# Optimization experiments

Measured on AMD Instinct MI355X. Metric: run time of the kernel, lower is better.

## Reference

```python
import jax, jax.numpy as jnp
import numpy as np

HID = 3584; NH = 16; NKV = 8; HD = 256; S = 3072; WIN = 2048
SOFTCAP = 50.0; QSCALE = 256.0 ** -0.5  # query_pre_attn_scalar = 256
NEG = -2.3819763e38


def _rope(x, cos, sin):
    # x: (B, S, heads, HD); cos/sin: (S, HD//2). Gemma half-split complex RoPE.
    x1, x2 = jnp.split(x, 2, axis=-1)
    c = cos[None, :, None, :]
    s = sin[None, :, None, :]
    return jnp.concatenate([x1 * c - x2 * s, x1 * s + x2 * c], axis=-1)


def setup_inputs() -> dict:
    key = jax.random.key(0)
    k1, k2, k3 = jax.random.split(key, 3)
    hidden_states = jax.random.normal(k1, (1, S, HID), jnp.float32)
    qkv_w = jax.random.normal(k2, (NH * HD + 2 * NKV * HD, HID), jnp.float32) * 0.02
    o_w = jax.random.normal(k3, (HID, NH * HD), jnp.float32) * 0.02
    inv = 1.0 / (10000.0 ** (jnp.arange(0, HD, 2, dtype=jnp.float32) / HD))
    ang = jnp.arange(S, dtype=jnp.float32)[:, None] * inv[None, :]
    freqs_cis = jnp.stack([jnp.cos(ang), jnp.sin(ang)], axis=-1)  # (S, HD//2, 2)
    kv_write_indices = jnp.arange(S, dtype=jnp.int32)
    k_cache = jnp.zeros((1, S, NKV, HD), jnp.float32)
    v_cache = jnp.zeros((1, S, NKV, HD), jnp.float32)
    i = jnp.arange(S)[:, None]
    j = jnp.arange(S)[None, :]
    mask = jnp.where(j <= i, 0.0, NEG).astype(jnp.float32)[None, None]  # causal (1,1,S,S)
    return dict(hidden_states=hidden_states, freqs_cis=freqs_cis,
                kv_write_indices=kv_write_indices, k_cache=k_cache, v_cache=v_cache,
                mask=mask, qkv_w=qkv_w, o_w=o_w)


def reference(hidden_states, freqs_cis, kv_write_indices, k_cache, v_cache, mask, qkv_w, o_w):
    B, L, _ = hidden_states.shape
    qkv = hidden_states @ qkv_w.T  # (B, L, 8192)
    xq, xk, xv = jnp.split(qkv, [NH * HD, NH * HD + NKV * HD], axis=-1)
    xq = xq.reshape(B, L, NH, HD)
    xk = xk.reshape(B, L, NKV, HD)
    xv = xv.reshape(B, L, NKV, HD)
    cos, sin = freqs_cis[..., 0], freqs_cis[..., 1]
    xq = _rope(xq, cos, sin)
    xk = _rope(xk, cos, sin)
    # KV cache index_copy_ on dim 1
    k_all = k_cache.at[:, kv_write_indices].set(xk)  # (B, T, NKV, HD)
    v_all = v_cache.at[:, kv_write_indices].set(xv)
    T = k_all.shape[1]
    G = NH // NKV  # queries per kv head; grouped einsum avoids repeat_interleave
    q = (xq * QSCALE).transpose(0, 2, 1, 3).reshape(B, NKV, G, L, HD)
    k = k_all.transpose(0, 2, 1, 3)  # (B, NKV, T, HD)
    v = v_all.transpose(0, 2, 1, 3)
    scores = jnp.einsum('bkgsd,bktd->bkgst', q, k)
    # logit softcapping
    scores = jnp.tanh(scores / SOFTCAP) * SOFTCAP
    # sliding-window band applied on top of the provided (causal) mask
    i = jnp.arange(L)[:, None]
    j = jnp.arange(T)[None, :]
    band = (j >= i - WIN + 1) & (j <= i + WIN - 1)
    m = jnp.where(band, mask, NEG)  # (1,1,L,T)
    scores = scores + m[:, :, None]  # broadcast over group dim
    probs = jax.nn.softmax(scores.astype(jnp.float32), axis=-1).astype(q.dtype)
    out = jnp.einsum('bkgst,bktd->bkgsd', probs, v)
    out = out.reshape(B, NH, L, HD).transpose(0, 2, 1, 3).reshape(B, L, NH * HD)
    return out @ o_w.T
```

## Files before the change

kernel.cpp:

```cpp
#include <hip/hip_runtime.h>

#define S_LEN 3072
#define NHQ 16
#define NKVH 8
#define HDIM 256
#define WIN 2048
#define QKV_COLS 8192

typedef __bf16 bf16x8 __attribute__((ext_vector_type(8)));
typedef float f32x4 __attribute__((ext_vector_type(4)));

__device__ __forceinline__ unsigned short f2bf(float f) {
    union { float f; unsigned u; } v; v.f = f;
    unsigned r = v.u + 0x7FFFu + ((v.u >> 16) & 1u);
    return (unsigned short)(r >> 16);
}
__device__ __forceinline__ float bf2f(unsigned short u) {
    union { unsigned u; float f; } v; v.u = ((unsigned)u) << 16; return v.f;
}

typedef __attribute__((address_space(3))) void lds_void_t;
typedef const __attribute__((address_space(1))) void glb_void_t;
__device__ __forceinline__ void async16(const void* g, void* l) {
    __builtin_amdgcn_global_load_lds((glb_void_t*)g, (lds_void_t*)l, 16, 0, 0);
}

__global__ __launch_bounds__(256) void cast_bf16_kernel(const float* __restrict__ src,
                                                        unsigned short* __restrict__ dst,
                                                        int n) {
    int i = (blockIdx.x * 256 + threadIdx.x) * 4;
    if (i >= n) return;
    float4 v = *(const float4*)(src + i);
    ushort4 o;
    o.x = f2bf(v.x); o.y = f2bf(v.y); o.z = f2bf(v.z); o.w = f2bf(v.w);
    *(ushort4*)(dst + i) = o;
}

template <int OUT_BF16>
__global__ __launch_bounds__(256) void gemm_bt(const unsigned short* __restrict__ A,
                                               const unsigned short* __restrict__ B,
                                               void* __restrict__ Cv,
                                               int N, int K) {
    __shared__ __align__(16) unsigned short At[128 * 32];
    __shared__ __align__(16) unsigned short Bt[128 * 32];
    const int tid = threadIdx.x;
    const int wid = tid >> 6, lane = tid & 63;
    const int ln = lane & 15, quad = lane >> 4;
    const int bm = blockIdx.y, bn = blockIdx.x;
    const int wm = wid >> 1, wn = wid & 1;

    const f32x4 fzero = {0.f, 0.f, 0.f, 0.f};
    f32x4 acc[4][4];
#pragma unroll
    for (int i = 0; i < 4; i++) {
#pragma unroll
        for (int j = 0; j < 4; j++) acc[i][j] = fzero;
    }

    const unsigned short* gA = A + (size_t)(bm * 128 + wid * 32 + (lane >> 2)) * K + (lane & 3) * 8;
    const unsigned short* gB = B + (size_t)(bn * 128 + wid * 32 + (lane >> 2)) * K + (lane & 3) * 8;
    unsigned short* lA = At + wid * 32 * 32;
    unsigned short* lB = Bt + wid * 32 * 32;

    for (int k0 = 0; k0 < K; k0 += 32) {
        async16(gA + k0, lA);
        async16(gA + k0 + 16 * K, lA + 16 * 32);
        async16(gB + k0, lB);
        async16(gB + k0 + 16 * K, lB + 16 * 32);
        __syncthreads();

        bf16x8 af[4], bfr[4];
#pragma unroll
        for (int mt = 0; mt < 4; mt++)
            af[mt] = *(const bf16x8*)(At + (wm * 64 + mt * 16 + ln) * 32 + quad * 8);
#pragma unroll
        for (int nt = 0; nt < 4; nt++)
            bfr[nt] = *(const bf16x8*)(Bt + (wn * 64 + nt * 16 + ln) * 32 + quad * 8);
#pragma unroll
        for (int mt = 0; mt < 4; mt++) {
#pragma unroll
            for (int nt = 0; nt < 4; nt++)
                acc[mt][nt] = __builtin_amdgcn_mfma_f32_16x16x32_bf16(af[mt], bfr[nt], acc[mt][nt], 0, 0, 0);
        }
        __syncthreads();
    }

    const int row0 = bm * 128 + wm * 64 + quad * 4;
    const int col0 = bn * 128 + wn * 64 + ln;
    if (OUT_BF16) {
        unsigned short* C = (unsigned short*)Cv;
#pragma unroll
        for (int mt = 0; mt < 4; mt++) {
#pragma unroll
            for (int nt = 0; nt < 4; nt++) {
#pragma unroll
                for (int rr = 0; rr < 4; rr++)
                    C[(size_t)(row0 + mt * 16 + rr) * N + col0 + nt * 16] = f2bf(acc[mt][nt][rr]);
            }
        }
    } else {
        float* C = (float*)Cv;
#pragma unroll
        for (int mt = 0; mt < 4; mt++) {
#pragma unroll
            for (int nt = 0; nt < 4; nt++) {
#pragma unroll
                for (int rr = 0; rr < 4; rr++)
                    C[(size_t)(row0 + mt * 16 + rr) * N + col0 + nt * 16] = acc[mt][nt][rr];
            }
        }
    }
}

__global__ __launch_bounds__(256) void rope_kernel(const unsigned short* __restrict__ qkv,
                                                   const float* __restrict__ freqs,
                                                   const int* __restrict__ kvidx,
                                                   unsigned short* __restrict__ Qb,
                                                   unsigned short* __restrict__ Kb) {
    int t = blockIdx.x * 256 + threadIdx.x;
    int d = t & 127;
    int t2 = t >> 7;
    int hh = t2 % 24;
    int pos = t2 / 24;
    if (pos >= S_LEN) return;
    float2 cs = *(const float2*)(freqs + ((size_t)pos * 128 + d) * 2);
    if (hh < NHQ) {
        const unsigned short* src = qkv + (size_t)pos * QKV_COLS + hh * HDIM + d;
        float x1 = bf2f(src[0]), x2 = bf2f(src[128]);
        float o1 = (x1 * cs.x - x2 * cs.y) * 0.0625f;
        float o2 = (x1 * cs.y + x2 * cs.x) * 0.0625f;
        unsigned short* dst = Qb + ((size_t)hh * S_LEN + pos) * HDIM + d;
        dst[0] = f2bf(o1);
        dst[128] = f2bf(o2);
    } else {
        int kvh = hh - NHQ;
        const unsigned short* src = qkv + (size_t)pos * QKV_COLS + NHQ * HDIM + kvh * HDIM + d;
        float x1 = bf2f(src[0]), x2 = bf2f(src[128]);
        float o1 = x1 * cs.x - x2 * cs.y;
        float o2 = x1 * cs.y + x2 * cs.x;
        int wpos = kvidx[pos];
        unsigned short* dst = Kb + ((size_t)kvh * S_LEN + wpos) * HDIM + d;
        dst[0] = f2bf(o1);
        dst[128] = f2bf(o2);
    }
}

__global__ __launch_bounds__(256) void vtrans_kernel(const unsigned short* __restrict__ qkv,
                                                     const int* __restrict__ kvidx,
                                                     unsigned short* __restrict__ Vbt) {
    __shared__ unsigned short T[64][72];
    int pos0 = blockIdx.x * 64;
    int c0 = blockIdx.y * 64;
    int a = threadIdx.x >> 6;
    int b = threadIdx.x & 63;
#pragma unroll
    for (int r = 0; r < 16; r++) {
        int pl = r * 4 + a;
        T[pl][b] = qkv[(size_t)(pos0 + pl) * QKV_COLS + 6144 + c0 + b];
    }
    __syncthreads();
    int wpos = kvidx[pos0 + b];
#pragma unroll
    for (int r = 0; r < 16; r++) {
        int cl = r * 4 + a;
        Vbt[(size_t)(c0 + cl) * S_LEN + wpos] = T[b][cl];
    }
}

__global__ __launch_bounds__(256) void attn_kernel(const unsigned short* __restrict__ Qb,
                                                   const unsigned short* __restrict__ Kb,
                                                   const unsigned short* __restrict__ Vbt,
                                                   float* __restrict__ Acc,
                                                   float* __restrict__ Ps,
                                                   unsigned short* __restrict__ attn_out) {
    __shared__ __align__(16) unsigned short Kl[32][264];
    __shared__ __align__(16) unsigned short Vt[256][40];
    __shared__ __align__(16) unsigned short Pl[4][16][40];

    const int h = blockIdx.x / 96;
    const int it = 95 - (blockIdx.x % 96);
    int qb, sub, nc;
    if (it < 16)      { qb = it; sub = 0; nc = 1; }
    else if (it < 48) { int e = it - 16; qb = 16 + (e >> 1); sub = e & 1; nc = 2; }
    else              { int e = it - 48; qb = 32 + e / 3; sub = e % 3; nc = 3; }

    const int kv = h >> 1;
    const int q0 = qb * 64;
    const int tid = threadIdx.x;
    const int wid = tid >> 6, lane = tid & 63;
    const int ln = lane & 15, quad = lane >> 4;

    bf16x8 qf[8];
    {
        const unsigned short* qrow = Qb + ((size_t)h * S_LEN + q0 + wid * 16 + ln) * HDIM;
#pragma unroll
        for (int k0 = 0; k0 < 8; k0++)
            qf[k0] = *(const bf16x8*)(qrow + k0 * 32 + quad * 8);
    }

    const f32x4 fzero = {0.f, 0.f, 0.f, 0.f};
    f32x4 acc[16];
#pragma unroll
    for (int t = 0; t < 16; t++) acc[t] = fzero;
    float ps[4] = {0.f, 0.f, 0.f, 0.f};

    const int imin = q0 + wid * 16;
    const int imax = imin + 15;
    const int irow = imin + quad * 4;

    const int t_lo = (q0 >= WIN) ? ((q0 - (WIN - 1)) >> 5) : 0;
    const int t_hi = (q0 + 63) >> 5;
    const int tn = t_hi - t_lo + 1;
    const int ts = t_lo + (tn * sub) / nc;
    const int te = t_lo + (tn * (sub + 1)) / nc;

    const int krow = tid >> 3, kcs = (tid & 7) * 32;
    const unsigned short* ksrc0 = Kb + ((size_t)kv * S_LEN + krow) * HDIM + kcs;
    const unsigned short* vsrc0 = Vbt + ((size_t)kv * HDIM + tid) * S_LEN;

    for (int tt = ts; tt < te; tt++) {
        const int p0 = tt * 32;
        {
            const unsigned short* ks = ksrc0 + (size_t)p0 * HDIM;
            unsigned short* kd = &Kl[krow][kcs];
#pragma unroll
            for (int j = 0; j < 4; j++)
                *(uint4*)(kd + j * 8) = *(const uint4*)(ks + j * 8);
            const unsigned short* vs = vsrc0 + p0;
            unsigned short* vd = &Vt[tid][0];
#pragma unroll
            for (int j = 0; j < 4; j++)
                *(uint4*)(vd + j * 8) = *(const uint4*)(vs + j * 8);
        }
        __syncthreads();

        const bool live = (p0 <= imax) && (p0 + 31 >= imin - WIN + 1);
        if (live) {
            f32x4 s0 = fzero, s1 = fzero;
#pragma unroll
            for (int k0 = 0; k0 < 8; k0++) {
                bf16x8 b0 = *(const bf16x8*)(&Kl[ln][k0 * 32 + quad * 8]);
                s0 = __builtin_amdgcn_mfma_f32_16x16x32_bf16(qf[k0], b0, s0, 0, 0, 0);
            }
#pragma unroll
            for (int k0 = 0; k0 < 8; k0++) {
                bf16x8 b1 = *(const bf16x8*)(&Kl[16 + ln][k0 * 32 + quad * 8]);
                s1 = __builtin_amdgcn_mfma_f32_16x16x32_bf16(qf[k0], b1, s1, 0, 0, 0);
            }

            const bool full = (p0 + 31 <= imin) && (p0 >= imax - WIN + 1);
#pragma unroll
            for (int r = 0; r < 4; r++) {
                float z0 = __expf(s0[r] * 0.04f);
                float z1 = __expf(s1[r] * 0.04f);
                float t0 = fmaf(-100.f, __builtin_amdgcn_rcpf(z0 + 1.f), 50.f);
                float t1 = fmaf(-100.f, __builtin_amdgcn_rcpf(z1 + 1.f), 50.f);
                float p0v = __expf(t0);
                float p1v = __expf(t1);
                if (!full) {
                    const int i = irow + r;
                    int j0 = p0 + ln, j1 = p0 + 16 + ln;
                    p0v = ((j0 <= i) && (j0 + WIN > i)) ? p0v : 0.f;
                    p1v = ((j1 <= i) && (j1 + WIN > i)) ? p1v : 0.f;
                }
                ps[r] += p0v + p1v;
                Pl[wid][quad * 4 + r][ln] = f2bf(p0v);
                Pl[wid][quad * 4 + r][16 + ln] = f2bf(p1v);
            }
            bf16x8 pa = *(const bf16x8*)(&Pl[wid][ln][quad * 8]);
#pragma unroll
            for (int t = 0; t < 16; t++) {
                bf16x8 vb = *(const bf16x8*)(&Vt[t * 16 + ln][quad * 8]);
                acc[t] = __builtin_amdgcn_mfma_f32_16x16x32_bf16(pa, vb, acc[t], 0, 0, 0);
            }
        }
        __syncthreads();
    }

    float psr[4];
#pragma unroll
    for (int r = 0; r < 4; r++) {
        float s = ps[r];
#pragma unroll
        for (int o = 1; o <= 8; o <<= 1)
            s += __shfl_xor(s, o);
        psr[r] = s;
    }

    if (nc == 1) {
#pragma unroll
        for (int t = 0; t < 16; t++) {
#pragma unroll
            for (int r = 0; r < 4; r++) {
                float o = acc[t][r] * __builtin_amdgcn_rcpf(psr[r]);
                attn_out[(size_t)(irow + r) * 4096 + h * HDIM + t * 16 + ln] = f2bf(o);
            }
        }
    } else {
        if (ln == 0) {
#pragma unroll
            for (int r = 0; r < 4; r++)
                atomicAdd(&Ps[h * S_LEN + irow + r], psr[r]);
        }
#pragma unroll
        for (int t = 0; t < 16; t++) {
#pragma unroll
            for (int r = 0; r < 4; r++)
                atomicAdd(&Acc[((size_t)h * S_LEN + irow + r) * HDIM + t * 16 + ln], acc[t][r]);
        }
    }
}

__global__ __launch_bounds__(256) void norm_kernel(const float* __restrict__ Acc,
                                                   const float* __restrict__ Ps,
                                                   unsigned short* __restrict__ attn_out) {
    int row = blockIdx.x * 4 + (threadIdx.x >> 6);
    int lane = threadIdx.x & 63;
    int h = row >> 11;
    int pos = 1024 + (row & 2047);
    float4 a = *(const float4*)(Acc + ((size_t)h * S_LEN + pos) * HDIM + lane * 4);
    float inv = __builtin_amdgcn_rcpf(Ps[h * S_LEN + pos]);
    ushort4 o;
    o.x = f2bf(a.x * inv); o.y = f2bf(a.y * inv);
    o.z = f2bf(a.z * inv); o.w = f2bf(a.w * inv);
    *(ushort4*)(attn_out + (size_t)pos * 4096 + h * HDIM + lane * 4) = o;
}

extern "C" void kernel_launch(void* const* d_in, const int* in_sizes, int n_in,
                              void* d_out, int out_size, void* d_ws, size_t ws_size,
                              hipStream_t stream) {
    (void)in_sizes; (void)n_in; (void)out_size; (void)ws_size;
    const float* hidden = (const float*)d_in[0];
    const float* freqs  = (const float*)d_in[1];
    const int* kvidx    = (const int*)d_in[2];
    const float* qkv_w  = (const float*)d_in[6];
    const float* o_w    = (const float*)d_in[7];
    float* out = (float*)d_out;

    char* ws = (char*)d_ws;
    unsigned short* hs_bf   = (unsigned short*)(ws);
    unsigned short* w1_bf   = (unsigned short*)(ws + 22020096);
    unsigned short* w2_bf   = (unsigned short*)(ws + 80740352);
    unsigned short* qkv_bf  = (unsigned short*)(ws + 110100480);
    unsigned short* Qb      = (unsigned short*)(ws + 160432128);
    unsigned short* Kb      = (unsigned short*)(ws + 185597952);
    unsigned short* Vbt     = (unsigned short*)(ws + 198180864);
    unsigned short* attn_bf = (unsigned short*)(ws + 210763776);

    float* Acc = (float*)(ws + 110100480);
    float* Ps  = (float*)(ws);

    cast_bf16_kernel<<<10752, 256, 0, stream>>>(hidden, hs_bf, 11010048);
    cast_bf16_kernel<<<28672, 256, 0, stream>>>(qkv_w, w1_bf, 29360128);
    cast_bf16_kernel<<<14336, 256, 0, stream>>>(o_w, w2_bf, 14680064);

    gemm_bt<1><<<dim3(64, 24), 256, 0, stream>>>(hs_bf, w1_bf, (void*)qkv_bf, 8192, 3584);

    rope_kernel<<<36864, 256, 0, stream>>>(qkv_bf, freqs, kvidx, Qb, Kb);
    vtrans_kernel<<<dim3(48, 32), 256, 0, stream>>>(qkv_bf, kvidx, Vbt);

    hipMemsetAsync(Acc, 0, (size_t)16 * 3072 * 256 * 4, stream);
    hipMemsetAsync(Ps, 0, (size_t)16 * 3072 * 4, stream);

    attn_kernel<<<1536, 256, 0, stream>>>(Qb, Kb, Vbt, Acc, Ps, attn_bf);
    norm_kernel<<<8192, 256, 0, stream>>>(Acc, Ps, attn_bf);

    gemm_bt<0><<<dim3(28, 24), 256, 0, stream>>>(attn_bf, w2_bf, (void*)out, 3584, 4096);
}
```

Measured before the change: 949.9 us.

## Share KV tiles across GQA head pair and double-buffer async LDS loads

The attention kernel now runs 512 threads per block so both query heads of a KV group share one K/V tile load, halving the block count and global K/V traffic. K/V tiles are fetched with async global-to-LDS loads into a double buffer, so the next tile's fetch overlaps the current tile's MFMA work and one barrier per iteration is removed. XOR swizzled LDS layouts replace the padded arrays to avoid bank conflicts. Larger blocks and the launch-bounds hint may reduce occupancy or raise register pressure.

New measurement: 943.2 us. About the same (-0.7%).

```diff
diff --git a/kernel.cpp b/kernel.cpp
--- a/kernel.cpp
+++ b/kernel.cpp
@@ -167,32 +167,33 @@
     }
 }
 
-__global__ __launch_bounds__(256) void attn_kernel(const unsigned short* __restrict__ Qb,
-                                                   const unsigned short* __restrict__ Kb,
-                                                   const unsigned short* __restrict__ Vbt,
-                                                   float* __restrict__ Acc,
-                                                   float* __restrict__ Ps,
-                                                   unsigned short* __restrict__ attn_out) {
-    __shared__ __align__(16) unsigned short Kl[32][264];
-    __shared__ __align__(16) unsigned short Vt[256][40];
-    __shared__ __align__(16) unsigned short Pl[4][16][40];
-
-    const int h = blockIdx.x / 96;
+__global__ __launch_bounds__(512, 4) void attn_kernel(const unsigned short* __restrict__ Qb,
+                                                      const unsigned short* __restrict__ Kb,
+                                                      const unsigned short* __restrict__ Vbt,
+                                                      float* __restrict__ Acc,
+                                                      float* __restrict__ Ps,
+                                                      unsigned short* __restrict__ attn_out) {
+    __shared__ __align__(16) unsigned short Kl[2][32 * 256];
+    __shared__ __align__(16) unsigned short Vl[2][256 * 32];
+    __shared__ __align__(16) unsigned short Plb[8][16][40];
+
+    const int kv = blockIdx.x / 96;
     const int it = 95 - (blockIdx.x % 96);
     int qb, sub, nc;
     if (it < 16)      { qb = it; sub = 0; nc = 1; }
     else if (it < 48) { int e = it - 16; qb = 16 + (e >> 1); sub = e & 1; nc = 2; }
     else              { int e = it - 48; qb = 32 + e / 3; sub = e % 3; nc = 3; }
 
-    const int kv = h >> 1;
     const int q0 = qb * 64;
     const int tid = threadIdx.x;
     const int wid = tid >> 6, lane = tid & 63;
     const int ln = lane & 15, quad = lane >> 4;
+    const int h = kv * 2 + (wid >> 2);
+    const int wrow = (wid & 3) * 16;
 
     bf16x8 qf[8];
     {
-        const unsigned short* qrow = Qb + ((size_t)h * S_LEN + q0 + wid * 16 + ln) * HDIM;
+        const unsigned short* qrow = Qb + ((size_t)h * S_LEN + q0 + wrow + ln) * HDIM;
 #pragma unroll
         for (int k0 = 0; k0 < 8; k0++)
             qf[k0] = *(const bf16x8*)(qrow + k0 * 32 + quad * 8);
@@ -204,7 +205,7 @@
     for (int t = 0; t < 16; t++) acc[t] = fzero;
     float ps[4] = {0.f, 0.f, 0.f, 0.f};
 
-    const int imin = q0 + wid * 16;
+    const int imin = q0 + wrow;
     const int imax = imin + 15;
     const int irow = imin + quad * 4;
 
@@ -214,37 +215,55 @@
     const int ts = t_lo + (tn * sub) / nc;
     const int te = t_lo + (tn * (sub + 1)) / nc;
 
-    const int krow = tid >> 3, kcs = (tid & 7) * 32;
-    const unsigned short* ksrc0 = Kb + ((size_t)kv * S_LEN + krow) * HDIM + kcs;
-    const unsigned short* vsrc0 = Vbt + ((size_t)kv * HDIM + tid) * S_LEN;
+    const unsigned short* kSrcA = Kb + ((size_t)kv * S_LEN + (tid >> 5)) * HDIM
+                                  + ((tid & 31) ^ ((tid >> 5) & 7)) * 8;
+    const unsigned short* vSrcA = Vbt + ((size_t)kv * HDIM + (tid >> 2)) * S_LEN
+                                  + ((tid & 3) ^ ((tid >> 3) & 3)) * 8;
+
+    {
+        const int p0s = ts * 32;
+        const unsigned short* ks = kSrcA + (size_t)p0s * HDIM;
+        const unsigned short* vs = vSrcA + p0s;
+        async16(ks,                 &Kl[0][tid * 8]);
+        async16(ks + 16 * HDIM,     &Kl[0][(512 + tid) * 8]);
+        async16(vs,                 &Vl[0][tid * 8]);
+        async16(vs + 128 * S_LEN,   &Vl[0][(512 + tid) * 8]);
+    }
+
+    const int kswz = (ln & 7);
+    const unsigned short* vbb_off = (const unsigned short*)0; (void)vbb_off;
+    int cur = 0;
 
     for (int tt = ts; tt < te; tt++) {
+        asm volatile("s_waitcnt vmcnt(0)" ::: "memory");
+        __builtin_amdgcn_s_barrier();
+        asm volatile("" ::: "memory");
+
+        if (tt + 1 < te) {
+            const int p0n = (tt + 1) * 32;
+            const unsigned short* ks = kSrcA + (size_t)p0n * HDIM;
+            const unsigned short* vs = vSrcA + p0n;
+            async16(ks,                 &Kl[cur ^ 1][tid * 8]);
+            async16(ks + 16 * HDIM,     &Kl[cur ^ 1][(512 + tid) * 8]);
+            async16(vs,                 &Vl[cur ^ 1][tid * 8]);
+            async16(vs + 128 * S_LEN,   &Vl[cur ^ 1][(512 + tid) * 8]);
+        }
+
         const int p0 = tt * 32;
-        {
-            const unsigned short* ks = ksrc0 + (size_t)p0 * HDIM;
-            unsigned short* kd = &Kl[krow][kcs];
-#pragma unroll
-            for (int j = 0; j < 4; j++)
-                *(uint4*)(kd + j * 8) = *(const uint4*)(ks + j * 8);
-            const unsigned short* vs = vsrc0 + p0;
-            unsigned short* vd = &Vt[tid][0];
-#pragma unroll
-            for (int j = 0; j < 4; j++)
-                *(uint4*)(vd + j * 8) = *(const uint4*)(vs + j * 8);
-        }
-        __syncthreads();
-
         const bool live = (p0 <= imax) && (p0 + 31 >= imin - WIN + 1);
         if (live) {
+            const unsigned short* kb = Kl[cur];
             f32x4 s0 = fzero, s1 = fzero;
 #pragma unroll
             for (int k0 = 0; k0 < 8; k0++) {
-                bf16x8 b0 = *(const bf16x8*)(&Kl[ln][k0 * 32 + quad * 8]);
+                const int cp = (((k0 * 4 + quad) ^ kswz) << 3);
+                bf16x8 b0 = *(const bf16x8*)(kb + ln * HDIM + cp);
                 s0 = __builtin_amdgcn_mfma_f32_16x16x32_bf16(qf[k0], b0, s0, 0, 0, 0);
             }
 #pragma unroll
             for (int k0 = 0; k0 < 8; k0++) {
-                bf16x8 b1 = *(const bf16x8*)(&Kl[16 + ln][k0 * 32 + quad * 8]);
+                const int cp = (((k0 * 4 + quad) ^ kswz) << 3);
+                bf16x8 b1 = *(const bf16x8*)(kb + (16 + ln) * HDIM + cp);
                 s1 = __builtin_amdgcn_mfma_f32_16x16x32_bf16(qf[k0], b1, s1, 0, 0, 0);
             }
 
@@ -264,17 +283,18 @@
                     p1v = ((j1 <= i) && (j1 + WIN > i)) ? p1v : 0.f;
                 }
                 ps[r] += p0v + p1v;
-                Pl[wid][quad * 4 + r][ln] = f2bf(p0v);
-                Pl[wid][quad * 4 + r][16 + ln] = f2bf(p1v);
-            }
-            bf16x8 pa = *(const bf16x8*)(&Pl[wid][ln][quad * 8]);
+                Plb[wid][quad * 4 + r][ln] = f2bf(p0v);
+                Plb[wid][quad * 4 + r][16 + ln] = f2bf(p1v);
+            }
+            bf16x8 pa = *(const bf16x8*)(&Plb[wid][ln][quad * 8]);
+            const unsigned short* vbb = Vl[cur] + ln * 32 + ((quad ^ ((ln >> 1) & 3)) << 3);
 #pragma unroll
             for (int t = 0; t < 16; t++) {
-                bf16x8 vb = *(const bf16x8*)(&Vt[t * 16 + ln][quad * 8]);
+                bf16x8 vb = *(const bf16x8*)(vbb + t * 512);
                 acc[t] = __builtin_amdgcn_mfma_f32_16x16x32_bf16(pa, vb, acc[t], 0, 0, 0);
             }
         }
-        __syncthreads();
+        cur ^= 1;
     }
 
     float psr[4];
@@ -362,7 +382,7 @@
     hipMemsetAsync(Acc, 0, (size_t)16 * 3072 * 256 * 4, stream);
     hipMemsetAsync(Ps, 0, (size_t)16 * 3072 * 4, stream);
 
-    attn_kernel<<<1536, 256, 0, stream>>>(Qb, Kb, Vbt, Acc, Ps, attn_bf);
+    attn_kernel<<<768, 512, 0, stream>>>(Qb, Kb, Vbt, Acc, Ps, attn_bf);
     norm_kernel<<<8192, 256, 0, stream>>>(Acc, Ps, attn_bf);
 
     gemm_bt<0><<<dim3(28, 24), 256, 0, stream>>>(attn_bf, w2_bf, (void*)out, 3584, 4096);
```
